# Kernel optimization log

Hardware: AMD Instinct MI355X
Metric: run time of the kernel (lower is better)

Reference implementation:

```python
import jax, jax.numpy as jnp
import numpy as np

N_NODES = 100000
NEG_SLOPE = 0.2  # PyG GATConv default LeakyReLU slope


def gat_conv(x, src, dst, W, a_src, a_dst, bias, n):
    # x: [N, Fin] -> h: [N, Fout]; heads=1, concat=True (PyG defaults), add_self_loops=False
    h = x @ W
    alpha_s = h @ a_src  # [N]
    alpha_d = h @ a_dst  # [N]
    e = jax.nn.leaky_relu(alpha_s[src] + alpha_d[dst], NEG_SLOPE)  # [E]
    # segment-softmax over edges grouped by destination node
    m = jax.ops.segment_max(e, dst, num_segments=n)  # [N], -inf for isolated nodes (never gathered)
    ex = jnp.exp(e - m[dst])
    denom = jax.ops.segment_sum(ex, dst, num_segments=n)
    alpha = ex / denom[dst]  # [E]
    out = jax.ops.segment_sum(alpha[:, None] * h[src], dst, num_segments=n)
    return out + bias


def setup_inputs() -> dict:
    key = jax.random.key(0)
    ks = jax.random.split(key, 12)
    n, e, fin, hid, ncls = N_NODES, 6400000, 128, 8, 16
    x = jax.random.normal(ks[0], (n, fin), dtype=jnp.float32)
    edge_index = jax.random.randint(ks[1], (2, e), 0, n, dtype=jnp.int32)
    s1 = 1.0 / np.sqrt(fin)
    s2 = 1.0 / np.sqrt(hid)
    return {
        "x": x,
        "edge_index": edge_index,
        "W1": jax.random.normal(ks[2], (fin, hid), dtype=jnp.float32) * s1,
        "a1_src": jax.random.normal(ks[3], (hid,), dtype=jnp.float32) * s2,
        "a1_dst": jax.random.normal(ks[4], (hid,), dtype=jnp.float32) * s2,
        "b1": jnp.zeros((hid,), dtype=jnp.float32),
        "W2": jax.random.normal(ks[5], (hid, ncls), dtype=jnp.float32) * s2,
        "a2_src": jax.random.normal(ks[6], (ncls,), dtype=jnp.float32) * 0.25,
        "a2_dst": jax.random.normal(ks[7], (ncls,), dtype=jnp.float32) * 0.25,
        "b2": jnp.zeros((ncls,), dtype=jnp.float32),
    }


def reference(x, edge_index, W1, a1_src, a1_dst, b1, W2, a2_src, a2_dst, b2):
    src, dst = edge_index[0], edge_index[1]
    n = x.shape[0]
    h = jax.nn.relu(gat_conv(x, src, dst, W1, a1_src, a1_dst, b1, n))
    # F.dropout(training=False) in inference -> identity
    out = gat_conv(h, src, dst, W2, a2_src, a2_dst, b2, n)
    return jax.nn.log_softmax(out, axis=1)
```

## Files before the change

### kernel.cpp

```cpp
#include <hip/hip_runtime.h>
#include <hip/hip_fp16.h>
#include <math.h>
#include <stdint.h>

#define NEG 0.2f
#define CSHIFT 9
#define BUCKN (1 << CSHIFT)
#define MAXNB 256
#define CHUNK 4096


__global__ __launch_bounds__(256) void k1_node(const float* __restrict__ x,
    const float* __restrict__ W1, const float* __restrict__ a1s, const float* __restrict__ a1d,
    float4* __restrict__ h1pk, float* __restrict__ ad1, int n)
{
    __shared__ float wt[8 * 128];
    __shared__ float av[16];
    for (int i = threadIdx.x; i < 1024; i += 256) {
        int r = i >> 3, k = i & 7;
        wt[k * 128 + r] = W1[i];
    }
    if (threadIdx.x < 8)        av[threadIdx.x] = a1s[threadIdx.x];
    else if (threadIdx.x < 16)  av[threadIdx.x] = a1d[threadIdx.x - 8];
    __syncthreads();

    int lane = threadIdx.x & 31;
    int node = blockIdx.x * 8 + (threadIdx.x >> 5);
    if (node >= n) return;

    float4 xv = ((const float4*)(x + (size_t)node * 128))[lane];
    float p[8];
#pragma unroll
    for (int k = 0; k < 8; ++k) {
        float4 wv = ((const float4*)(wt + k * 128))[lane];
        p[k] = xv.x * wv.x + xv.y * wv.y + xv.z * wv.z + xv.w * wv.w;
    }
#pragma unroll
    for (int off = 16; off; off >>= 1)
#pragma unroll
        for (int k = 0; k < 8; ++k) p[k] += __shfl_down(p[k], off, 32);

    if (lane == 0) {
        float s = 0.f, d = 0.f;
        union { float4 f; __half2 h[4]; } u;
#pragma unroll
        for (int k = 0; k < 8; ++k) {
            s += p[k] * av[k];
            d += p[k] * av[8 + k];
        }
#pragma unroll
        for (int q = 0; q < 4; ++q) u.h[q] = __floats2half2_rn(p[2 * q], p[2 * q + 1]);
        h1pk[2 * (size_t)node]     = u.f;
        h1pk[2 * (size_t)node + 1] = make_float4(s, 0.f, 0.f, 0.f);
        ad1[node] = d;
    }
}


__global__ __launch_bounds__(256) void p1a(const int* __restrict__ dst, int* __restrict__ gmat,
                                           int E, int NB)
{
    __shared__ int h[MAXNB];
    for (int i = threadIdx.x; i < NB; i += 256) h[i] = 0;
    __syncthreads();
    int base = blockIdx.x * CHUNK;
    int end = base + CHUNK; if (end > E) end = E;
    for (int i = base + threadIdx.x; i < end; i += 256)
        atomicAdd(&h[dst[i] >> CSHIFT], 1);
    __syncthreads();
    int* row = gmat + (size_t)blockIdx.x * NB;
    for (int i = threadIdx.x; i < NB; i += 256) row[i] = h[i];
}

__global__ __launch_bounds__(256) void pcol(const int* __restrict__ gmat, int* __restrict__ pbaseRel,
    int* __restrict__ total, int NBLK, int NB)
{
    __shared__ int wsum[4];
    int b = blockIdx.x;
    int tid = threadIdx.x;
    int chunk = (NBLK + 255) >> 8;
    int k0 = tid * chunk;
    int s = 0;
    for (int j = 0; j < chunk; ++j) {
        int k = k0 + j;
        if (k < NBLK) s += gmat[(size_t)k * NB + b];
    }
    int lane = tid & 63, w = tid >> 6;
    int sc = s;
#pragma unroll
    for (int off = 1; off < 64; off <<= 1) {
        int t = __shfl_up(sc, off, 64);
        if (lane >= off) sc += t;
    }
    if (lane == 63) wsum[w] = sc;
    __syncthreads();
    if (tid == 0) { int a = 0; for (int i = 0; i < 4; ++i) { int t = wsum[i]; wsum[i] = a; a += t; } }
    __syncthreads();
    int run = sc - s + wsum[w];
    for (int j = 0; j < chunk; ++j) {
        int k = k0 + j;
        if (k < NBLK) {
            int gv = gmat[(size_t)k * NB + b];
            pbaseRel[(size_t)k * NB + b] = run;
            run += gv;
        }
    }
    if (tid == 255) total[b] = run;
}

__global__ __launch_bounds__(512) void ptot(const int* __restrict__ total, int* __restrict__ cptr,
                                            int* __restrict__ row_ptr, int NB, int n, int E)
{
    __shared__ int wsum[8];
    int b = threadIdx.x;
    int v = b < NB ? total[b] : 0;
    int lane = b & 63, w = b >> 6;
    int s = v;
#pragma unroll
    for (int off = 1; off < 64; off <<= 1) {
        int t = __shfl_up(s, off, 64);
        if (lane >= off) s += t;
    }
    if (lane == 63) wsum[w] = s;
    __syncthreads();
    if (b == 0) { int a = 0; for (int i = 0; i < 8; ++i) { int t = wsum[i]; wsum[i] = a; a += t; } }
    __syncthreads();
    int excl = s - v + wsum[w];
    if (b < NB) cptr[b] = excl;
    if (b == 0) { cptr[NB] = E; row_ptr[n] = E; }
}

__global__ __launch_bounds__(256) void p1bW(const int* __restrict__ src, const int* __restrict__ dst,
    const int* __restrict__ gmat, const int* __restrict__ cptr, const int* __restrict__ pbaseRel,
    unsigned* __restrict__ stage, int E, int NB)
{
    __shared__ int lbase[MAXNB], bbase[MAXNB], ccur[MAXNB];
    __shared__ unsigned bufp[CHUNK];
    __shared__ unsigned short bufb[CHUNK];
    __shared__ int wsum[4];
    int tid = threadIdx.x;
    if (tid < NB) ccur[tid] = 0;

    int base = blockIdx.x * CHUNK;
    int end = base + CHUNK; if (end > E) end = E;
    int cnt = end - base;

    int v = (tid < NB) ? gmat[(size_t)blockIdx.x * NB + tid] : 0;
    int lane = tid & 63, w = tid >> 6;
    int sc = v;
#pragma unroll
    for (int off = 1; off < 64; off <<= 1) {
        int t = __shfl_up(sc, off, 64);
        if (lane >= off) sc += t;
    }
    if (lane == 63) wsum[w] = sc;
    __syncthreads();
    if (tid == 0) { int a = 0; for (int i = 0; i < 4; ++i) { int t = wsum[i]; wsum[i] = a; a += t; } }
    __syncthreads();
    if (tid < NB) {
        lbase[tid] = sc - v + wsum[w];
        bbase[tid] = cptr[tid] + pbaseRel[(size_t)blockIdx.x * NB + tid];
    }
    __syncthreads();

    for (int i = base + tid; i < end; i += 256) {
        int d = dst[i];
        int b = d >> CSHIFT;
        int off = atomicAdd(&ccur[b], 1);
        int pos = lbase[b] + off;
        bufp[pos] = ((unsigned)(d & (BUCKN - 1)) << 17) | (unsigned)src[i];
        bufb[pos] = (unsigned short)b;
    }
    __syncthreads();

    for (int i = tid; i < cnt; i += 256) {
        int b = bufb[i];
        stage[bbase[b] + (i - lbase[b])] = bufp[i];
    }
}

__global__ __launch_bounds__(512) void p2(const unsigned* __restrict__ stage,
    const int* __restrict__ cptr, int* __restrict__ colsrc, int* __restrict__ row_ptr, int n)
{
    int b = blockIdx.x;
    int nbase = b << CSHIFT;
    int NN = n - nbase; if (NN > BUCKN) NN = BUCKN;
    __shared__ int h[BUCKN], bps[BUCKN], cc[BUCKN];
    __shared__ int wsum[8];
    int tid = threadIdx.x;
    h[tid] = 0; cc[tid] = 0;
    __syncthreads();
    int s0 = cptr[b], s1 = cptr[b + 1];
    for (int i = s0 + tid; i < s1; i += 512)
        atomicAdd(&h[stage[i] >> 17], 1);
    __syncthreads();
    int v = h[tid];
    int lane = tid & 63, w = tid >> 6;
    int sc = v;
#pragma unroll
    for (int off = 1; off < 64; off <<= 1) {
        int t = __shfl_up(sc, off, 64);
        if (lane >= off) sc += t;
    }
    if (lane == 63) wsum[w] = sc;
    __syncthreads();
    if (tid == 0) { int a = 0; for (int i = 0; i < 8; ++i) { int t = wsum[i]; wsum[i] = a; a += t; } }
    __syncthreads();
    int excl = sc - v + wsum[w];
    bps[tid] = s0 + excl;
    if (tid < NN) row_ptr[nbase + tid] = s0 + excl;
    __syncthreads();
    for (int i = s0 + tid; i < s1; i += 512) {
        unsigned p = stage[i];
        int f = p >> 17;
        int off = atomicAdd(&cc[f], 1);
        colsrc[bps[f] + off] = (int)(p & 0x1FFFFu);
    }
}


__global__ __launch_bounds__(256) void k_gather8f(const int* __restrict__ row_ptr,
    const int* __restrict__ colsrc, const float4* __restrict__ featpk, const float* __restrict__ ad,
    const float* __restrict__ b1, const float* __restrict__ W2,
    const float* __restrict__ a2s, const float* __restrict__ a2d,
    float4* __restrict__ outpk, float* __restrict__ ad2, int n)
{
    __shared__ float w2as[8], w2ad[8], b1v[8];
    if (threadIdx.x < 8) {
        float s = 0.f, d = 0.f;
#pragma unroll
        for (int c = 0; c < 16; ++c) {
            float wv = W2[threadIdx.x * 16 + c];
            s += wv * a2s[c];
            d += wv * a2d[c];
        }
        w2as[threadIdx.x] = s;
        w2ad[threadIdx.x] = d;
        b1v[threadIdx.x] = b1[threadIdx.x];
    }
    __syncthreads();

    int wid  = (blockIdx.x * 256 + threadIdx.x) >> 6;
    int lane = threadIdx.x & 63;
    int l16  = lane & 15;
    int node = wid * 4 + (lane >> 4);
    bool active = node < n;

    int start = 0, end = 0;
    float adn = 0.f;
    if (active) { start = row_ptr[node]; end = row_ptr[node + 1]; adn = ad[node]; }

    float wsum = 0.f, acc[8];
#pragma unroll
    for (int k = 0; k < 8; ++k) acc[k] = 0.f;

    for (int i = start + l16; i < end; i += 16) {
        int s = colsrc[i];
        union { float4 fv; __half2 h[4]; } u;
        u.fv = featpk[2 * (size_t)s];
        float4 meta = featpk[2 * (size_t)s + 1];
        float t = meta.x + adn;
        float w = __expf(t > 0.f ? t : NEG * t);
        wsum += w;
#pragma unroll
        for (int q = 0; q < 4; ++q) {
            float2 hv = __half22float2(u.h[q]);
            acc[2 * q + 0] += w * hv.x;
            acc[2 * q + 1] += w * hv.y;
        }
    }
#pragma unroll
    for (int off = 8; off; off >>= 1) {
        wsum += __shfl_xor(wsum, off, 64);
#pragma unroll
        for (int k = 0; k < 8; ++k) acc[k] += __shfl_xor(acc[k], off, 64);
    }
    if (!active || l16 != 0) return;

    float inv = wsum > 0.f ? 1.f / wsum : 0.f;
    float h[8], s2 = 0.f, d2 = 0.f;
    union { float4 f; __half2 hh[4]; } u;
#pragma unroll
    for (int k = 0; k < 8; ++k) {
        float v = acc[k] * inv + b1v[k];
        h[k] = v > 0.f ? v : 0.f;
        s2 += h[k] * w2as[k];
        d2 += h[k] * w2ad[k];
    }
#pragma unroll
    for (int q = 0; q < 4; ++q) u.hh[q] = __floats2half2_rn(h[2 * q], h[2 * q + 1]);
    outpk[2 * (size_t)node]     = u.f;
    outpk[2 * (size_t)node + 1] = make_float4(s2, 0.f, 0.f, 0.f);
    ad2[node] = d2;
}

__global__ __launch_bounds__(256) void k_gather16(const int* __restrict__ row_ptr,
    const int* __restrict__ colsrc, const float4* __restrict__ featpk, const float* __restrict__ ad,
    const float* __restrict__ W2, const float* __restrict__ bias, float* __restrict__ outp, int n)
{
    __shared__ float w2s[128], bv[16];
    if (threadIdx.x < 128) w2s[threadIdx.x] = W2[threadIdx.x];
    else if (threadIdx.x < 144) bv[threadIdx.x - 128] = bias[threadIdx.x - 128];
    __syncthreads();

    int wid  = (blockIdx.x * 256 + threadIdx.x) >> 6;
    int lane = threadIdx.x & 63;
    int l16  = lane & 15;
    int node = wid * 4 + (lane >> 4);
    bool active = node < n;

    int start = 0, end = 0;
    float adn = 0.f;
    if (active) { start = row_ptr[node]; end = row_ptr[node + 1]; adn = ad[node]; }

    float wsum = 0.f, acc[8];
#pragma unroll
    for (int k = 0; k < 8; ++k) acc[k] = 0.f;

    for (int i = start + l16; i < end; i += 16) {
        int s = colsrc[i];
        union { float4 fv; __half2 h[4]; } u;
        u.fv = featpk[2 * (size_t)s];
        float4 meta = featpk[2 * (size_t)s + 1];
        float t = meta.x + adn;
        float w = __expf(t > 0.f ? t : NEG * t);
        wsum += w;
#pragma unroll
        for (int q = 0; q < 4; ++q) {
            float2 hv = __half22float2(u.h[q]);
            acc[2 * q + 0] += w * hv.x;
            acc[2 * q + 1] += w * hv.y;
        }
    }
#pragma unroll
    for (int off = 8; off; off >>= 1) {
        wsum += __shfl_xor(wsum, off, 64);
#pragma unroll
        for (int k = 0; k < 8; ++k) acc[k] += __shfl_xor(acc[k], off, 64);
    }
    if (!active) return;

    float inv = wsum > 0.f ? 1.f / wsum : 0.f;
    float o = bv[l16];
#pragma unroll
    for (int k = 0; k < 8; ++k) o += (acc[k] * inv) * w2s[k * 16 + l16];
    float m = o;
#pragma unroll
    for (int off = 8; off; off >>= 1) m = fmaxf(m, __shfl_xor(m, off, 64));
    float se = __expf(o - m);
#pragma unroll
    for (int off = 8; off; off >>= 1) se += __shfl_xor(se, off, 64);
    float l = m + __logf(se);
    outp[(size_t)node * 16 + l16] = o - l;
}


__global__ __launch_bounds__(256) void k1_nodeF(const float* __restrict__ x,
    const float* __restrict__ W1, const float* __restrict__ a1s, const float* __restrict__ a1d,
    float* __restrict__ h1, float* __restrict__ as1, float* __restrict__ ad1, int n)
{
    __shared__ float wt[8 * 128];
    __shared__ float av[16];
    for (int i = threadIdx.x; i < 1024; i += 256) {
        int r = i >> 3, k = i & 7;
        wt[k * 128 + r] = W1[i];
    }
    if (threadIdx.x < 8)        av[threadIdx.x] = a1s[threadIdx.x];
    else if (threadIdx.x < 16)  av[threadIdx.x] = a1d[threadIdx.x - 8];
    __syncthreads();

    int lane = threadIdx.x & 31;
    int node = blockIdx.x * 8 + (threadIdx.x >> 5);
    if (node >= n) return;

    float4 xv = ((const float4*)(x + (size_t)node * 128))[lane];
    float p[8];
#pragma unroll
    for (int k = 0; k < 8; ++k) {
        float4 wv = ((const float4*)(wt + k * 128))[lane];
        p[k] = xv.x * wv.x + xv.y * wv.y + xv.z * wv.z + xv.w * wv.w;
    }
#pragma unroll
    for (int off = 16; off; off >>= 1)
#pragma unroll
        for (int k = 0; k < 8; ++k) p[k] += __shfl_down(p[k], off, 32);

    if (lane == 0) {
        float s = 0.f, d = 0.f;
#pragma unroll
        for (int k = 0; k < 8; ++k) {
            h1[(size_t)node * 8 + k] = p[k];
            s += p[k] * av[k];
            d += p[k] * av[8 + k];
        }
        as1[node] = s;
        ad1[node] = d;
    }
}

template <int F>
__global__ __launch_bounds__(256) void k_edge(const int* __restrict__ src, const int* __restrict__ dst,
    const float* __restrict__ as, const float* __restrict__ ad, const float* __restrict__ feat,
    float* __restrict__ denom, float* __restrict__ acc, int E)
{
    int e = blockIdx.x * 256 + threadIdx.x;
    if (e >= E) return;
    int s = src[e], d = dst[e];
    float t = as[s] + ad[d];
    float w = __expf(t > 0.f ? t : NEG * t);
    atomicAdd(denom + d, w);
    const float* fs = feat + (size_t)s * F;
    float* ac = acc + (size_t)d * F;
#pragma unroll
    for (int k = 0; k < F; ++k) atomicAdd(ac + k, w * fs[k]);
}

__global__ __launch_bounds__(256) void k3_node(const float* __restrict__ denom1,
    const float* __restrict__ acc1, const float* __restrict__ b1,
    const float* __restrict__ W2, const float* __restrict__ a2s, const float* __restrict__ a2d,
    float* __restrict__ g, float* __restrict__ as2, float* __restrict__ ad2, int n)
{
    __shared__ float w2[128];
    __shared__ float aa[32];
    __shared__ float bb[8];
    if (threadIdx.x < 128) w2[threadIdx.x] = W2[threadIdx.x];
    if (threadIdx.x >= 128 && threadIdx.x < 144) aa[threadIdx.x - 128] = a2s[threadIdx.x - 128];
    if (threadIdx.x >= 144 && threadIdx.x < 160) aa[16 + threadIdx.x - 144] = a2d[threadIdx.x - 144];
    if (threadIdx.x >= 160 && threadIdx.x < 168) bb[threadIdx.x - 160] = b1[threadIdx.x - 160];
    __syncthreads();

    int node = blockIdx.x * 256 + threadIdx.x;
    if (node >= n) return;
    float dn = denom1[node];
    float inv = dn > 0.f ? 1.f / dn : 0.f;
    float h[8];
#pragma unroll
    for (int k = 0; k < 8; ++k) {
        float v = acc1[(size_t)node * 8 + k] * inv + bb[k];
        h[k] = v > 0.f ? v : 0.f;
    }
    float s = 0.f, dd = 0.f;
#pragma unroll
    for (int c = 0; c < 16; ++c) {
        float gv = 0.f;
#pragma unroll
        for (int k = 0; k < 8; ++k) gv += h[k] * w2[k * 16 + c];
        g[(size_t)node * 16 + c] = gv;
        s += gv * aa[c];
        dd += gv * aa[16 + c];
    }
    as2[node] = s;
    ad2[node] = dd;
}

__global__ __launch_bounds__(256) void k5_final(const float* __restrict__ denom2,
    const float* __restrict__ acc2, const float* __restrict__ b2, float* __restrict__ out, int n)
{
    __shared__ float bb[16];
    if (threadIdx.x < 16) bb[threadIdx.x] = b2[threadIdx.x];
    __syncthreads();

    int node = blockIdx.x * 256 + threadIdx.x;
    if (node >= n) return;
    float dn = denom2[node];
    float inv = dn > 0.f ? 1.f / dn : 0.f;
    float o[16];
    float m = -1e30f;
#pragma unroll
    for (int c = 0; c < 16; ++c) {
        o[c] = acc2[(size_t)node * 16 + c] * inv + bb[c];
        m = fmaxf(m, o[c]);
    }
    float se = 0.f;
#pragma unroll
    for (int c = 0; c < 16; ++c) {
        o[c] -= m;
        se += __expf(o[c]);
    }
    float l = __logf(se);
#pragma unroll
    for (int c = 0; c < 16; ++c) out[(size_t)node * 16 + c] = o[c] - l;
}


static inline char* align256(char* p) {
    return (char*)(((uintptr_t)p + 255) & ~(uintptr_t)255);
}

extern "C" void kernel_launch(void* const* d_in, const int* in_sizes, int n_in,
                              void* d_out, int out_size, void* d_ws, size_t ws_size,
                              hipStream_t stream)
{
    const float* x    = (const float*)d_in[0];
    const int*   eidx = (const int*)d_in[1];
    const float* W1   = (const float*)d_in[2];
    const float* a1s  = (const float*)d_in[3];
    const float* a1d  = (const float*)d_in[4];
    const float* b1   = (const float*)d_in[5];
    const float* W2   = (const float*)d_in[6];
    const float* a2s  = (const float*)d_in[7];
    const float* a2d  = (const float*)d_in[8];
    const float* b2   = (const float*)d_in[9];
    float* out = (float*)d_out;

    const int n = in_sizes[0] / 128;
    const int E = in_sizes[1] / 2;
    const int* src = eidx;
    const int* dst = eidx + E;
    const int NB = (n + BUCKN - 1) >> CSHIFT;
    const int NBLK = (E + CHUNK - 1) / CHUNK;

    {
        char* p = (char*)d_ws;
        char* p0 = p;
        unsigned* stage = (unsigned*)p;  p = align256(p + (size_t)E * 4);
        int* colsrc  = (int*)p;          p = align256(p + (size_t)E * 4);
        int* total   = (int*)p;          p = align256(p + (size_t)NB * 4);
        int* cptr    = (int*)p;          p = align256(p + (size_t)(NB + 1) * 4);
        int* row_ptr = (int*)p;          p = align256(p + (size_t)(n + 1) * 4);
        float4* h1pk  = (float4*)p;      p = align256(p + (size_t)n * 32);
        float4* h1ppk = (float4*)p;      p = align256(p + (size_t)n * 32);
        float* ad1   = (float*)p;        p = align256(p + (size_t)n * 4);
        float* ad2   = (float*)p;        p = align256(p + (size_t)n * 4);
        size_t needed = (size_t)(p - p0);

        int* gmat     = colsrc;
        int* pbaseRel = (int*)align256((char*)(colsrc + (size_t)NBLK * NB));

        bool alias_ok = ((size_t)2 * NBLK * NB + 64) <= (size_t)E;

        if (n <= 131072 && NB <= MAXNB && alias_ok && ws_size >= needed) {
            k1_node<<<(n + 7) / 8, 256, 0, stream>>>(x, W1, a1s, a1d, h1pk, ad1, n);

            p1a<<<NBLK, 256, 0, stream>>>(dst, gmat, E, NB);
            pcol<<<NB, 256, 0, stream>>>(gmat, pbaseRel, total, NBLK, NB);
            ptot<<<1, 512, 0, stream>>>(total, cptr, row_ptr, NB, n, E);
            p1bW<<<NBLK, 256, 0, stream>>>(src, dst, gmat, cptr, pbaseRel, stage, E, NB);
            p2<<<NB, 512, 0, stream>>>(stage, cptr, colsrc, row_ptr, n);

            const int gblocks = ((size_t)n * 16 + 255) / 256;
            k_gather8f<<<gblocks, 256, 0, stream>>>(row_ptr, colsrc, h1pk, ad1,
                                                    b1, W2, a2s, a2d, h1ppk, ad2, n);
            k_gather16<<<gblocks, 256, 0, stream>>>(row_ptr, colsrc, h1ppk, ad2, W2, b2, out, n);
            return;
        }
    }

    {
        float* ws     = (float*)d_ws;
        float* denom1 = ws;
        float* acc1   = ws + (size_t)n;
        float* denom2 = ws + (size_t)9 * n;
        float* acc2   = ws + (size_t)10 * n;
        float* h1     = ws + (size_t)26 * n;
        float* as1    = ws + (size_t)34 * n;
        float* ad1    = ws + (size_t)35 * n;
        float* g      = ws + (size_t)36 * n;
        float* as2    = ws + (size_t)52 * n;
        float* ad2    = ws + (size_t)53 * n;

        hipMemsetAsync(ws, 0, (size_t)26 * n * sizeof(float), stream);
        k1_nodeF<<<(n + 7) / 8, 256, 0, stream>>>(x, W1, a1s, a1d, h1, as1, ad1, n);
        k_edge<8><<<(E + 255) / 256, 256, 0, stream>>>(src, dst, as1, ad1, h1, denom1, acc1, E);
        k3_node<<<(n + 255) / 256, 256, 0, stream>>>(denom1, acc1, b1, W2, a2s, a2d, g, as2, ad2, n);
        k_edge<16><<<(E + 255) / 256, 256, 0, stream>>>(src, dst, as2, ad2, g, denom2, acc2, E);
        k5_final<<<(n + 255) / 256, 256, 0, stream>>>(denom2, acc2, b2, out, n);
    }
}
```

Before: 219.1 us.

## Shrink CSR buckets to 128 nodes and stage bucket scatter in LDS

Reduces the node bucket size from 512 to 128, so there are more buckets (up to 1024). The prefix-scan kernels become chunked per thread to handle more buckets than threads. The per-bucket scatter in p2 now builds its output in a shared-memory buffer and writes colsrc contiguously, falling back to direct global scatter when a bucket overflows the buffer. This aims at more p2 blocks for parallelism and coalesced colsrc writes, but p1bW must track 4x more bucket bases per chunk and emits smaller, more fragmented stage writes.

```diff
diff --git a/kernel.cpp b/kernel.cpp
--- a/kernel.cpp
+++ b/kernel.cpp
@@ -4,10 +4,11 @@
 #include <stdint.h>
 
 #define NEG 0.2f
-#define CSHIFT 9
+#define CSHIFT 7
 #define BUCKN (1 << CSHIFT)
-#define MAXNB 256
+#define MAXNB 1024
 #define CHUNK 4096
+#define FBUF 9216
 
 
 __global__ __launch_bounds__(256) void k1_node(const float* __restrict__ x,
@@ -112,22 +113,31 @@
                                             int* __restrict__ row_ptr, int NB, int n, int E)
 {
     __shared__ int wsum[8];
-    int b = threadIdx.x;
-    int v = b < NB ? total[b] : 0;
-    int lane = b & 63, w = b >> 6;
-    int s = v;
+    int tid = threadIdx.x;
+    int chunk = (NB + 511) >> 9;
+    int k0 = tid * chunk;
+    int s = 0;
+    for (int j = 0; j < chunk; ++j) {
+        int k = k0 + j;
+        if (k < NB) s += total[k];
+    }
+    int lane = tid & 63, w = tid >> 6;
+    int sc = s;
 #pragma unroll
     for (int off = 1; off < 64; off <<= 1) {
-        int t = __shfl_up(s, off, 64);
-        if (lane >= off) s += t;
-    }
-    if (lane == 63) wsum[w] = s;
-    __syncthreads();
-    if (b == 0) { int a = 0; for (int i = 0; i < 8; ++i) { int t = wsum[i]; wsum[i] = a; a += t; } }
-    __syncthreads();
-    int excl = s - v + wsum[w];
-    if (b < NB) cptr[b] = excl;
-    if (b == 0) { cptr[NB] = E; row_ptr[n] = E; }
+        int t = __shfl_up(sc, off, 64);
+        if (lane >= off) sc += t;
+    }
+    if (lane == 63) wsum[w] = sc;
+    __syncthreads();
+    if (tid == 0) { int a = 0; for (int i = 0; i < 8; ++i) { int t = wsum[i]; wsum[i] = a; a += t; } }
+    __syncthreads();
+    int run = sc - s + wsum[w];
+    for (int j = 0; j < chunk; ++j) {
+        int k = k0 + j;
+        if (k < NB) { cptr[k] = run; run += total[k]; }
+    }
+    if (tid == 0) { cptr[NB] = E; row_ptr[n] = E; }
 }
 
 __global__ __launch_bounds__(256) void p1bW(const int* __restrict__ src, const int* __restrict__ dst,
@@ -139,15 +149,22 @@
     __shared__ unsigned short bufb[CHUNK];
     __shared__ int wsum[4];
     int tid = threadIdx.x;
-    if (tid < NB) ccur[tid] = 0;
+    const int* grow = gmat + (size_t)blockIdx.x * NB;
+    const int* prow = pbaseRel + (size_t)blockIdx.x * NB;
 
     int base = blockIdx.x * CHUNK;
     int end = base + CHUNK; if (end > E) end = E;
     int cnt = end - base;
 
-    int v = (tid < NB) ? gmat[(size_t)blockIdx.x * NB + tid] : 0;
+    int chunkb = (NB + 255) >> 8;
+    int b0 = tid * chunkb;
+    int s = 0;
+    for (int j = 0; j < chunkb; ++j) {
+        int b = b0 + j;
+        if (b < NB) s += grow[b];
+    }
     int lane = tid & 63, w = tid >> 6;
-    int sc = v;
+    int sc = s;
 #pragma unroll
     for (int off = 1; off < 64; off <<= 1) {
         int t = __shfl_up(sc, off, 64);
@@ -157,9 +174,15 @@
     __syncthreads();
     if (tid == 0) { int a = 0; for (int i = 0; i < 4; ++i) { int t = wsum[i]; wsum[i] = a; a += t; } }
     __syncthreads();
-    if (tid < NB) {
-        lbase[tid] = sc - v + wsum[w];
-        bbase[tid] = cptr[tid] + pbaseRel[(size_t)blockIdx.x * NB + tid];
+    int run = sc - s + wsum[w];
+    for (int j = 0; j < chunkb; ++j) {
+        int b = b0 + j;
+        if (b < NB) {
+            lbase[b] = run;
+            run += grow[b];
+            bbase[b] = cptr[b] + prow[b];
+            ccur[b] = 0;
+        }
     }
     __syncthreads();
 
@@ -186,35 +209,55 @@
     int nbase = b << CSHIFT;
     int NN = n - nbase; if (NN > BUCKN) NN = BUCKN;
     __shared__ int h[BUCKN], bps[BUCKN], cc[BUCKN];
-    __shared__ int wsum[8];
+    __shared__ int wsum[2];
+    __shared__ int buf[FBUF];
     int tid = threadIdx.x;
-    h[tid] = 0; cc[tid] = 0;
+    if (tid < BUCKN) { h[tid] = 0; cc[tid] = 0; }
     __syncthreads();
     int s0 = cptr[b], s1 = cptr[b + 1];
+    int span = s1 - s0;
     for (int i = s0 + tid; i < s1; i += 512)
         atomicAdd(&h[stage[i] >> 17], 1);
     __syncthreads();
-    int v = h[tid];
-    int lane = tid & 63, w = tid >> 6;
-    int sc = v;
-#pragma unroll
-    for (int off = 1; off < 64; off <<= 1) {
-        int t = __shfl_up(sc, off, 64);
-        if (lane >= off) sc += t;
-    }
-    if (lane == 63) wsum[w] = sc;
-    __syncthreads();
-    if (tid == 0) { int a = 0; for (int i = 0; i < 8; ++i) { int t = wsum[i]; wsum[i] = a; a += t; } }
-    __syncthreads();
-    int excl = sc - v + wsum[w];
-    bps[tid] = s0 + excl;
-    if (tid < NN) row_ptr[nbase + tid] = s0 + excl;
-    __syncthreads();
-    for (int i = s0 + tid; i < s1; i += 512) {
-        unsigned p = stage[i];
-        int f = p >> 17;
-        int off = atomicAdd(&cc[f], 1);
-        colsrc[bps[f] + off] = (int)(p & 0x1FFFFu);
+    if (tid < BUCKN) {
+        int v = h[tid];
+        int lane = tid & 63, w = tid >> 6;
+        int sc = v;
+#pragma unroll
+        for (int off = 1; off < 64; off <<= 1) {
+            int t = __shfl_up(sc, off, 64);
+            if (lane >= off) sc += t;
+        }
+        if (lane == 63) wsum[w] = sc;
+        __syncthreads();
+        if (tid == 0) { int a = 0; for (int i = 0; i < 2; ++i) { int t = wsum[i]; wsum[i] = a; a += t; } }
+        __syncthreads();
+        int excl = sc - v + wsum[w];
+        bps[tid] = excl;
+        if (tid < NN) row_ptr[nbase + tid] = s0 + excl;
+    } else {
+        __syncthreads();
+        __syncthreads();
+    }
+    __syncthreads();
+
+    if (span <= FBUF) {
+        for (int i = s0 + tid; i < s1; i += 512) {
+            unsigned p = stage[i];
+            int f = p >> 17;
+            int off = atomicAdd(&cc[f], 1);
+            buf[bps[f] + off] = (int)(p & 0x1FFFFu);
+        }
+        __syncthreads();
+        for (int i = tid; i < span; i += 512)
+            colsrc[s0 + i] = buf[i];
+    } else {
+        for (int i = s0 + tid; i < s1; i += 512) {
+            unsigned p = stage[i];
+            int f = p >> 17;
+            int off = atomicAdd(&cc[f], 1);
+            colsrc[s0 + bps[f] + off] = (int)(p & 0x1FFFFu);
+        }
     }
 }
 
```

Result: no change. 215.3 us (-1.7%).
